# Optimization experiments

Measured on AMD Instinct MI355X. Metric: run time of the kernel, lower is better.

## Reference

```python
import jax, jax.numpy as jnp
import numpy as np

B = 131072   # batch
D = 128      # input_dim
H = 512      # hidden_dim
E = 2        # number of tasks/experts (fixed in module)
O = 2        # output dim (fixed in module)


def setup_inputs() -> dict:
    key = jax.random.key(0)
    k0, k1, k2, k3 = jax.random.split(key, 4)
    x = jax.random.normal(k0, (B, D), jnp.float32)
    # kaiming-uniform-ish scale for weights
    w1 = jax.random.normal(k1, (E, H, D), jnp.float32) * (1.0 / np.sqrt(D).astype(np.float32))
    b1 = jnp.zeros((E, H), jnp.float32)
    w2 = jax.random.normal(k2, (E, O, H), jnp.float32) * (1.0 / np.sqrt(H).astype(np.float32))
    b2 = jnp.zeros((E, O), jnp.float32)
    # buffer is zeros in torch; randomize so routing is non-degenerate
    prototypes = jax.random.normal(k3, (E, D), jnp.float32)
    return {"x": x, "w1": w1, "b1": b1, "w2": w2, "b2": b2, "prototypes": prototypes}


def reference(x, w1, b1, w2, b2, prototypes):
    # Routing: torch.cdist -> argmin. Squared distance has the same argmin
    # as euclidean distance (sqrt is monotone), so skip the sqrt.
    diff = x[:, None, :] - prototypes[None, :, :]          # [B, E, D]
    d2 = jnp.sum(diff * diff, axis=-1)                     # [B, E]
    t = jnp.argmin(d2, axis=1)                             # [B] int

    # Only E=2 experts: evaluate both and select, instead of a per-sample
    # gathered [B,H,D] weight tensor (this replaces the torch python loop).
    h = jax.nn.relu(jnp.einsum('bd,ehd->beh', x, w1) + b1[None])   # [B, E, H]
    out_all = jnp.einsum('beh,eoh->beo', h, w2) + b2[None]          # [B, E, O]
    out = jnp.take_along_axis(out_all, t[:, None, None], axis=1)[:, 0, :]  # [B, O]
    return out
```

## Files before the change

### kernel.cpp

```cpp
#include <hip/hip_runtime.h>

typedef __bf16 bf16x8 __attribute__((ext_vector_type(8)));
typedef float floatx4 __attribute__((ext_vector_type(4)));

#define XS 136

__device__ __forceinline__ unsigned short f32_bf16(float f) {
    union { float f; unsigned int u; } c; c.f = f;
    return (unsigned short)((c.u + 0x7fffu + ((c.u >> 16) & 1u)) >> 16);
}

__global__ __launch_bounds__(256) void prep_w1_frag(const float* __restrict__ w1,
                                                    unsigned short* __restrict__ wbf) {
    int g    = blockIdx.x * 256 + threadIdx.x;
    int lane = g & 63;
    int frag = g >> 6;
    int ks   = frag & 3;
    int nt   = (frag >> 2) & 31;
    int e    = frag >> 7;
    int l15  = lane & 15;
    int quad = lane >> 4;
    const float* src = w1 + ((e * 512 + nt * 16 + l15) * 128 + ks * 32 + quad * 8);
    unsigned short* dst = wbf + (long)g * 8;
    #pragma unroll
    for (int j = 0; j < 8; ++j) dst[j] = f32_bf16(src[j]);
}

__global__ __launch_bounds__(256, 4) void moe_fused(
    const float* __restrict__ x,
    const unsigned short* __restrict__ wbf,
    const float* __restrict__ b1,
    const float* __restrict__ w2,
    const float* __restrict__ b2,
    const float* __restrict__ protos,
    float* __restrict__ out)
{
    __shared__ unsigned short xs[128 * XS];
    __shared__ float out_s[128 * 4];
    __shared__ int   t_s[128];

    const int tid  = threadIdx.x;
    const int lane = tid & 63;
    const int wave = tid >> 6;
    const int quad = lane >> 4;
    const int l15  = lane & 15;
    const int mh   = wave & 1;
    const int nh   = wave >> 1;
    const long rowbase = (long)blockIdx.x * 128;

    for (int i = tid; i < 128 * 32; i += 256) {
        int r  = i >> 5;
        int c4 = (i & 31) * 4;
        float4 v = *(const float4*)(x + (rowbase + r) * 128 + c4);
        ushort4 p;
        p.x = f32_bf16(v.x); p.y = f32_bf16(v.y);
        p.z = f32_bf16(v.z); p.w = f32_bf16(v.w);
        *(ushort4*)&xs[r * XS + c4] = p;
    }
    __syncthreads();

    {
        const int sub = tid & 15;
        const int e   = sub >> 3;
        const int j   = sub & 7;
        const float* pr = protos + e * 128;
        for (int rb = 0; rb < 128; rb += 16) {
            int r = rb + (tid >> 4);
            const float* xr = x + (rowbase + r) * 128;
            double acc = 0.0;
            #pragma unroll
            for (int k = 0; k < 16; ++k) {
                int c = j + 8 * k;
                double d = (double)xr[c] - (double)pr[c];
                acc = fma(d, d, acc);
            }
            acc += __shfl_xor(acc, 1);
            acc += __shfl_xor(acc, 2);
            acc += __shfl_xor(acc, 4);
            double other = __shfl_xor(acc, 8);
            if (sub == 0) t_s[r] = (other < acc) ? 1 : 0;
        }
    }

    bf16x8 afrag[4][4];
    #pragma unroll
    for (int mt = 0; mt < 4; ++mt) {
        int r = mh * 64 + mt * 16 + l15;
        #pragma unroll
        for (int ks = 0; ks < 4; ++ks)
            afrag[mt][ks] = *(const bf16x8*)&xs[r * XS + ks * 32 + quad * 8];
    }

    float outp[4][4][2] = {};

    const bf16x8* wb8 = (const bf16x8*)wbf + (long)(nh * 32) * 4 * 64 + lane;
    for (int nt = 0; nt < 32; ++nt) {
        const bf16x8* wp = wb8 + nt * 4 * 64;
        bf16x8 bf0 = wp[0];
        bf16x8 bf1 = wp[64];
        bf16x8 bf2 = wp[128];
        bf16x8 bf3 = wp[192];
        int hcol  = nt * 16 + l15;
        float bb  = b1[nh * 512 + hcol];
        float w2a = w2[(nh * 2 + 0) * 512 + hcol];
        float w2b = w2[(nh * 2 + 1) * 512 + hcol];
        #pragma unroll
        for (int mt = 0; mt < 4; ++mt) {
            floatx4 c = {bb, bb, bb, bb};
            c = __builtin_amdgcn_mfma_f32_16x16x32_bf16(afrag[mt][0], bf0, c, 0, 0, 0);
            c = __builtin_amdgcn_mfma_f32_16x16x32_bf16(afrag[mt][1], bf1, c, 0, 0, 0);
            c = __builtin_amdgcn_mfma_f32_16x16x32_bf16(afrag[mt][2], bf2, c, 0, 0, 0);
            c = __builtin_amdgcn_mfma_f32_16x16x32_bf16(afrag[mt][3], bf3, c, 0, 0, 0);
            #pragma unroll
            for (int rg = 0; rg < 4; ++rg) {
                float h = fmaxf(c[rg], 0.0f);
                outp[mt][rg][0] = fmaf(h, w2a, outp[mt][rg][0]);
                outp[mt][rg][1] = fmaf(h, w2b, outp[mt][rg][1]);
            }
        }
    }

    #pragma unroll
    for (int mt = 0; mt < 4; ++mt)
        #pragma unroll
        for (int rg = 0; rg < 4; ++rg)
            #pragma unroll
            for (int o = 0; o < 2; ++o) {
                float v = outp[mt][rg][o];
                v += __shfl_xor(v, 1);
                v += __shfl_xor(v, 2);
                v += __shfl_xor(v, 4);
                v += __shfl_xor(v, 8);
                outp[mt][rg][o] = v;
            }
    if (l15 == 0) {
        #pragma unroll
        for (int mt = 0; mt < 4; ++mt)
            #pragma unroll
            for (int rg = 0; rg < 4; ++rg) {
                int r = mh * 64 + mt * 16 + quad * 4 + rg;
                out_s[r * 4 + nh * 2 + 0] = outp[mt][rg][0];
                out_s[r * 4 + nh * 2 + 1] = outp[mt][rg][1];
            }
    }
    __syncthreads();

    {
        int r  = tid >> 1;
        int o  = tid & 1;
        int te = t_s[r];
        out[(rowbase + r) * 2 + o] = out_s[r * 4 + te * 2 + o] + b2[te * 2 + o];
    }
}

extern "C" void kernel_launch(void* const* d_in, const int* in_sizes, int n_in,
                              void* d_out, int out_size, void* d_ws, size_t ws_size,
                              hipStream_t stream) {
    const float* x      = (const float*)d_in[0];
    const float* w1     = (const float*)d_in[1];
    const float* b1     = (const float*)d_in[2];
    const float* w2     = (const float*)d_in[3];
    const float* b2     = (const float*)d_in[4];
    const float* protos = (const float*)d_in[5];
    float* out = (float*)d_out;
    unsigned short* wbf = (unsigned short*)d_ws;

    prep_w1_frag<<<dim3(64), dim3(256), 0, stream>>>(w1, wbf);
    moe_fused<<<dim3(1024), dim3(256), 0, stream>>>(x, wbf, b1, w2, b2, protos, out);
}
```

Baseline: 158.9 us.

## Halve block row tile, permute hidden columns for vector bias loads, linearize routing

Each block now handles 64 rows instead of 128, and the grid grows to 2048 blocks. This cuts per-wave fragment and accumulator registers and shared memory, which should allow more blocks per CU and better latency hiding. Hidden units are permuted in the weight prep so that each lane's b1/w2 values are contiguous, letting them load as float4 every four tiles. Routing is rewritten as a single linear discriminant, (a-b)·((a+b)/2 - x), computed with vectorized loads before the x staging rather than as two distance sums. The trade-off is that each block reuses the W1 fragments over fewer rows, so more L2 weight traffic is needed per row.

```diff
diff --git a/kernel.cpp b/kernel.cpp
--- a/kernel.cpp
+++ b/kernel.cpp
@@ -20,7 +20,8 @@
     int e    = frag >> 7;
     int l15  = lane & 15;
     int quad = lane >> 4;
-    const float* src = w1 + ((e * 512 + nt * 16 + l15) * 128 + ks * 32 + quad * 8);
+    int h    = l15 * 32 + nt;
+    const float* src = w1 + ((e * 512 + h) * 128 + ks * 32 + quad * 8);
     unsigned short* dst = wbf + (long)g * 8;
     #pragma unroll
     for (int j = 0; j < 8; ++j) dst[j] = f32_bf16(src[j]);
@@ -35,9 +36,9 @@
     const float* __restrict__ protos,
     float* __restrict__ out)
 {
-    __shared__ unsigned short xs[128 * XS];
-    __shared__ float out_s[128 * 4];
-    __shared__ int   t_s[128];
+    __shared__ unsigned short xs[64 * XS];
+    __shared__ float out_s[64 * 4];
+    __shared__ int   t_s[64];
 
     const int tid  = threadIdx.x;
     const int lane = tid & 63;
@@ -46,9 +47,31 @@
     const int l15  = lane & 15;
     const int mh   = wave & 1;
     const int nh   = wave >> 1;
-    const long rowbase = (long)blockIdx.x * 128;
+    const long rowbase = (long)blockIdx.x * 64;
 
-    for (int i = tid; i < 128 * 32; i += 256) {
+    {
+        int r   = tid >> 2;
+        int sub = tid & 3;
+        const float* xr = x + (rowbase + r) * 128 + sub * 32;
+        const float* p0 = protos + sub * 32;
+        const float* p1 = protos + 128 + sub * 32;
+        double acc = 0.0;
+        #pragma unroll
+        for (int k = 0; k < 8; ++k) {
+            float4 xv = *(const float4*)(xr + k * 4);
+            float4 a  = *(const float4*)(p0 + k * 4);
+            float4 b  = *(const float4*)(p1 + k * 4);
+            acc += ((double)a.x - b.x) * (0.5 * ((double)a.x + b.x) - xv.x);
+            acc += ((double)a.y - b.y) * (0.5 * ((double)a.y + b.y) - xv.y);
+            acc += ((double)a.z - b.z) * (0.5 * ((double)a.z + b.z) - xv.z);
+            acc += ((double)a.w - b.w) * (0.5 * ((double)a.w + b.w) - xv.w);
+        }
+        acc += __shfl_xor(acc, 1);
+        acc += __shfl_xor(acc, 2);
+        if (sub == 0) t_s[r] = (acc > 0.0) ? 1 : 0;
+    }
+
+    for (int i = tid; i < 64 * 32; i += 256) {
         int r  = i >> 5;
         int c4 = (i & 31) * 4;
         float4 v = *(const float4*)(x + (rowbase + r) * 128 + c4);
@@ -59,69 +82,54 @@
     }
     __syncthreads();
 
-    {
-        const int sub = tid & 15;
-        const int e   = sub >> 3;
-        const int j   = sub & 7;
-        const float* pr = protos + e * 128;
-        for (int rb = 0; rb < 128; rb += 16) {
-            int r = rb + (tid >> 4);
-            const float* xr = x + (rowbase + r) * 128;
-            double acc = 0.0;
-            #pragma unroll
-            for (int k = 0; k < 16; ++k) {
-                int c = j + 8 * k;
-                double d = (double)xr[c] - (double)pr[c];
-                acc = fma(d, d, acc);
-            }
-            acc += __shfl_xor(acc, 1);
-            acc += __shfl_xor(acc, 2);
-            acc += __shfl_xor(acc, 4);
-            double other = __shfl_xor(acc, 8);
-            if (sub == 0) t_s[r] = (other < acc) ? 1 : 0;
-        }
-    }
-
-    bf16x8 afrag[4][4];
+    bf16x8 afrag[2][4];
     #pragma unroll
-    for (int mt = 0; mt < 4; ++mt) {
-        int r = mh * 64 + mt * 16 + l15;
+    for (int mt = 0; mt < 2; ++mt) {
+        int r = mh * 32 + mt * 16 + l15;
         #pragma unroll
         for (int ks = 0; ks < 4; ++ks)
             afrag[mt][ks] = *(const bf16x8*)&xs[r * XS + ks * 32 + quad * 8];
     }
 
-    float outp[4][4][2] = {};
+    float outp[2][4][2] = {};
 
-    const bf16x8* wb8 = (const bf16x8*)wbf + (long)(nh * 32) * 4 * 64 + lane;
-    for (int nt = 0; nt < 32; ++nt) {
-        const bf16x8* wp = wb8 + nt * 4 * 64;
-        bf16x8 bf0 = wp[0];
-        bf16x8 bf1 = wp[64];
-        bf16x8 bf2 = wp[128];
-        bf16x8 bf3 = wp[192];
-        int hcol  = nt * 16 + l15;
-        float bb  = b1[nh * 512 + hcol];
-        float w2a = w2[(nh * 2 + 0) * 512 + hcol];
-        float w2b = w2[(nh * 2 + 1) * 512 + hcol];
+    const bf16x8* wb8 = (const bf16x8*)wbf + (long)nh * 32 * 4 * 64 + lane;
+    const float*  b1p = b1 + nh * 512 + l15 * 32;
+    const float*  w2ap = w2 + (nh * 2 + 0) * 512 + l15 * 32;
+    const float*  w2bp = w2 + (nh * 2 + 1) * 512 + l15 * 32;
+    for (int nt4 = 0; nt4 < 32; nt4 += 4) {
+        float4 bbv  = *(const float4*)(b1p  + nt4);
+        float4 w2av = *(const float4*)(w2ap + nt4);
+        float4 w2bv = *(const float4*)(w2bp + nt4);
         #pragma unroll
-        for (int mt = 0; mt < 4; ++mt) {
-            floatx4 c = {bb, bb, bb, bb};
-            c = __builtin_amdgcn_mfma_f32_16x16x32_bf16(afrag[mt][0], bf0, c, 0, 0, 0);
-            c = __builtin_amdgcn_mfma_f32_16x16x32_bf16(afrag[mt][1], bf1, c, 0, 0, 0);
-            c = __builtin_amdgcn_mfma_f32_16x16x32_bf16(afrag[mt][2], bf2, c, 0, 0, 0);
-            c = __builtin_amdgcn_mfma_f32_16x16x32_bf16(afrag[mt][3], bf3, c, 0, 0, 0);
+        for (int u = 0; u < 4; ++u) {
+            const bf16x8* wp = wb8 + (nt4 + u) * 256;
+            bf16x8 bf0 = wp[0];
+            bf16x8 bf1 = wp[64];
+            bf16x8 bf2 = wp[128];
+            bf16x8 bf3 = wp[192];
+            float bb  = ((const float*)&bbv)[u];
+            float w2a = ((const float*)&w2av)[u];
+            float w2b = ((const float*)&w2bv)[u];
             #pragma unroll
-            for (int rg = 0; rg < 4; ++rg) {
-                float h = fmaxf(c[rg], 0.0f);
-                outp[mt][rg][0] = fmaf(h, w2a, outp[mt][rg][0]);
-                outp[mt][rg][1] = fmaf(h, w2b, outp[mt][rg][1]);
+            for (int mt = 0; mt < 2; ++mt) {
+                floatx4 c = {bb, bb, bb, bb};
+                c = __builtin_amdgcn_mfma_f32_16x16x32_bf16(afrag[mt][0], bf0, c, 0, 0, 0);
+                c = __builtin_amdgcn_mfma_f32_16x16x32_bf16(afrag[mt][1], bf1, c, 0, 0, 0);
+                c = __builtin_amdgcn_mfma_f32_16x16x32_bf16(afrag[mt][2], bf2, c, 0, 0, 0);
+                c = __builtin_amdgcn_mfma_f32_16x16x32_bf16(afrag[mt][3], bf3, c, 0, 0, 0);
+                #pragma unroll
+                for (int rg = 0; rg < 4; ++rg) {
+                    float h = fmaxf(c[rg], 0.0f);
+                    outp[mt][rg][0] = fmaf(h, w2a, outp[mt][rg][0]);
+                    outp[mt][rg][1] = fmaf(h, w2b, outp[mt][rg][1]);
+                }
             }
         }
     }
 
     #pragma unroll
-    for (int mt = 0; mt < 4; ++mt)
+    for (int mt = 0; mt < 2; ++mt)
         #pragma unroll
         for (int rg = 0; rg < 4; ++rg)
             #pragma unroll
@@ -135,17 +143,17 @@
             }
     if (l15 == 0) {
         #pragma unroll
-        for (int mt = 0; mt < 4; ++mt)
+        for (int mt = 0; mt < 2; ++mt)
             #pragma unroll
             for (int rg = 0; rg < 4; ++rg) {
-                int r = mh * 64 + mt * 16 + quad * 4 + rg;
+                int r = mh * 32 + mt * 16 + quad * 4 + rg;
                 out_s[r * 4 + nh * 2 + 0] = outp[mt][rg][0];
                 out_s[r * 4 + nh * 2 + 1] = outp[mt][rg][1];
             }
     }
     __syncthreads();
 
-    {
+    if (tid < 128) {
         int r  = tid >> 1;
         int o  = tid & 1;
         int te = t_s[r];
@@ -166,5 +174,5 @@
     unsigned short* wbf = (unsigned short*)d_ws;
 
     prep_w1_frag<<<dim3(64), dim3(256), 0, stream>>>(w1, wbf);
-    moe_fused<<<dim3(1024), dim3(256), 0, stream>>>(x, wbf, b1, w2, b2, protos, out);
+    moe_fused<<<dim3(2048), dim3(256), 0, stream>>>(x, wbf, b1, w2, b2, protos, out);
 }
```

Result: slower. 172.4 us (+8.5%).

## Split hidden dim across waves, reuse each weight fragment over all 128 rows

Applied to the files above, without the earlier changes.

Each wave now covers all 128 rows of the block and half of the hidden units of one expert, so every loaded W1 fragment feeds 8 row tiles instead of 4. This halves the per-wave weight traffic, at the cost of twice as many A-fragment and accumulator registers. Launch bounds drop to 2 blocks per SIMD to fit those registers, which reduces occupancy. The W1 prep permutes hidden indices so that b1 and w2 loads become contiguous per lane. The routing test is rewritten as one linear test on the difference of the two prototypes, with float4 loads, and moved before the bf16 staging.

```diff
diff --git a/kernel.cpp b/kernel.cpp
--- a/kernel.cpp
+++ b/kernel.cpp
@@ -20,13 +20,14 @@
     int e    = frag >> 7;
     int l15  = lane & 15;
     int quad = lane >> 4;
-    const float* src = w1 + ((e * 512 + nt * 16 + l15) * 128 + ks * 32 + quad * 8);
+    int h    = l15 * 32 + nt;
+    const float* src = w1 + ((e * 512 + h) * 128 + ks * 32 + quad * 8);
     unsigned short* dst = wbf + (long)g * 8;
     #pragma unroll
     for (int j = 0; j < 8; ++j) dst[j] = f32_bf16(src[j]);
 }
 
-__global__ __launch_bounds__(256, 4) void moe_fused(
+__global__ __launch_bounds__(256, 2) void moe_fused(
     const float* __restrict__ x,
     const unsigned short* __restrict__ wbf,
     const float* __restrict__ b1,
@@ -36,17 +37,38 @@
     float* __restrict__ out)
 {
     __shared__ unsigned short xs[128 * XS];
-    __shared__ float out_s[128 * 4];
+    __shared__ float out_s[2][128][2][2];
     __shared__ int   t_s[128];
 
-    const int tid  = threadIdx.x;
-    const int lane = tid & 63;
-    const int wave = tid >> 6;
-    const int quad = lane >> 4;
-    const int l15  = lane & 15;
-    const int mh   = wave & 1;
-    const int nh   = wave >> 1;
+    const int tid   = threadIdx.x;
+    const int lane  = tid & 63;
+    const int wave  = tid >> 6;
+    const int quad  = lane >> 4;
+    const int l15   = lane & 15;
+    const int slice = wave & 1;
+    const int e     = wave >> 1;
     const long rowbase = (long)blockIdx.x * 128;
+
+    {
+        int r   = tid >> 1;
+        int sub = tid & 1;
+        const float* xr = x + (rowbase + r) * 128 + sub * 64;
+        const float* p0 = protos + sub * 64;
+        const float* p1 = protos + 128 + sub * 64;
+        double acc = 0.0;
+        #pragma unroll
+        for (int k = 0; k < 16; ++k) {
+            float4 xv = *(const float4*)(xr + k * 4);
+            float4 a  = *(const float4*)(p0 + k * 4);
+            float4 b  = *(const float4*)(p1 + k * 4);
+            acc += ((double)a.x - b.x) * (0.5 * ((double)a.x + b.x) - xv.x);
+            acc += ((double)a.y - b.y) * (0.5 * ((double)a.y + b.y) - xv.y);
+            acc += ((double)a.z - b.z) * (0.5 * ((double)a.z + b.z) - xv.z);
+            acc += ((double)a.w - b.w) * (0.5 * ((double)a.w + b.w) - xv.w);
+        }
+        acc += __shfl_xor(acc, 1);
+        if (sub == 0) t_s[r] = (acc > 0.0) ? 1 : 0;
+    }
 
     for (int i = tid; i < 128 * 32; i += 256) {
         int r  = i >> 5;
@@ -59,53 +81,33 @@
     }
     __syncthreads();
 
-    {
-        const int sub = tid & 15;
-        const int e   = sub >> 3;
-        const int j   = sub & 7;
-        const float* pr = protos + e * 128;
-        for (int rb = 0; rb < 128; rb += 16) {
-            int r = rb + (tid >> 4);
-            const float* xr = x + (rowbase + r) * 128;
-            double acc = 0.0;
-            #pragma unroll
-            for (int k = 0; k < 16; ++k) {
-                int c = j + 8 * k;
-                double d = (double)xr[c] - (double)pr[c];
-                acc = fma(d, d, acc);
-            }
-            acc += __shfl_xor(acc, 1);
-            acc += __shfl_xor(acc, 2);
-            acc += __shfl_xor(acc, 4);
-            double other = __shfl_xor(acc, 8);
-            if (sub == 0) t_s[r] = (other < acc) ? 1 : 0;
-        }
-    }
-
-    bf16x8 afrag[4][4];
+    bf16x8 afrag[8][4];
     #pragma unroll
-    for (int mt = 0; mt < 4; ++mt) {
-        int r = mh * 64 + mt * 16 + l15;
+    for (int mt = 0; mt < 8; ++mt) {
+        int r = mt * 16 + l15;
         #pragma unroll
         for (int ks = 0; ks < 4; ++ks)
             afrag[mt][ks] = *(const bf16x8*)&xs[r * XS + ks * 32 + quad * 8];
     }
 
-    float outp[4][4][2] = {};
+    float outp[8][4][2] = {};
 
-    const bf16x8* wb8 = (const bf16x8*)wbf + (long)(nh * 32) * 4 * 64 + lane;
-    for (int nt = 0; nt < 32; ++nt) {
-        const bf16x8* wp = wb8 + nt * 4 * 64;
+    const bf16x8* wb8 = (const bf16x8*)wbf + (long)((e * 32 + slice * 16) * 4) * 64 + lane;
+    const int    coff = e * 512 + l15 * 32 + slice * 16;
+    const float* b1p  = b1 + coff;
+    const float* w2ap = w2 + e * 1024 + l15 * 32 + slice * 16;
+    const float* w2bp = w2ap + 512;
+    for (int nt = 0; nt < 16; ++nt) {
+        const bf16x8* wp = wb8 + nt * 256;
         bf16x8 bf0 = wp[0];
         bf16x8 bf1 = wp[64];
         bf16x8 bf2 = wp[128];
         bf16x8 bf3 = wp[192];
-        int hcol  = nt * 16 + l15;
-        float bb  = b1[nh * 512 + hcol];
-        float w2a = w2[(nh * 2 + 0) * 512 + hcol];
-        float w2b = w2[(nh * 2 + 1) * 512 + hcol];
+        float bb  = b1p[nt];
+        float w2a = w2ap[nt];
+        float w2b = w2bp[nt];
         #pragma unroll
-        for (int mt = 0; mt < 4; ++mt) {
+        for (int mt = 0; mt < 8; ++mt) {
             floatx4 c = {bb, bb, bb, bb};
             c = __builtin_amdgcn_mfma_f32_16x16x32_bf16(afrag[mt][0], bf0, c, 0, 0, 0);
             c = __builtin_amdgcn_mfma_f32_16x16x32_bf16(afrag[mt][1], bf1, c, 0, 0, 0);
@@ -121,35 +123,29 @@
     }
 
     #pragma unroll
-    for (int mt = 0; mt < 4; ++mt)
+    for (int mt = 0; mt < 8; ++mt)
         #pragma unroll
-        for (int rg = 0; rg < 4; ++rg)
-            #pragma unroll
-            for (int o = 0; o < 2; ++o) {
-                float v = outp[mt][rg][o];
-                v += __shfl_xor(v, 1);
-                v += __shfl_xor(v, 2);
-                v += __shfl_xor(v, 4);
-                v += __shfl_xor(v, 8);
-                outp[mt][rg][o] = v;
+        for (int rg = 0; rg < 4; ++rg) {
+            float v0 = outp[mt][rg][0];
+            float v1 = outp[mt][rg][1];
+            v0 += __shfl_xor(v0, 1);  v1 += __shfl_xor(v1, 1);
+            v0 += __shfl_xor(v0, 2);  v1 += __shfl_xor(v1, 2);
+            v0 += __shfl_xor(v0, 4);  v1 += __shfl_xor(v1, 4);
+            v0 += __shfl_xor(v0, 8);  v1 += __shfl_xor(v1, 8);
+            if (l15 == 0) {
+                int r = mt * 16 + quad * 4 + rg;
+                out_s[slice][r][e][0] = v0;
+                out_s[slice][r][e][1] = v1;
             }
-    if (l15 == 0) {
-        #pragma unroll
-        for (int mt = 0; mt < 4; ++mt)
-            #pragma unroll
-            for (int rg = 0; rg < 4; ++rg) {
-                int r = mh * 64 + mt * 16 + quad * 4 + rg;
-                out_s[r * 4 + nh * 2 + 0] = outp[mt][rg][0];
-                out_s[r * 4 + nh * 2 + 1] = outp[mt][rg][1];
-            }
-    }
+        }
     __syncthreads();
 
     {
         int r  = tid >> 1;
         int o  = tid & 1;
         int te = t_s[r];
-        out[(rowbase + r) * 2 + o] = out_s[r * 4 + te * 2 + o] + b2[te * 2 + o];
+        out[(rowbase + r) * 2 + o] =
+            out_s[0][r][te][o] + out_s[1][r][te][o] + b2[te * 2 + o];
     }
 }
 
```

After: 158.3 us. Within noise of the previous version (-0.3%).
